# Kernel tuning notes

Hardware: AMD Instinct MI355X
Metric: run time of the kernel (lower is better)

## Reference

```python
import jax, jax.numpy as jnp
import numpy as np

WIN_SIZE = 256
PATCH_SIZE = [8]
CHANNEL = 32
B_CH = 256        # B_outer(8) * CHANNEL(32)
H, E = 8, 64


def _attn(q, k):
    # q, k: [B*ch, L, H, E] -> softmax scores [B*ch, H, L, L]
    scale = 1.0 / jnp.sqrt(jnp.asarray(E, q.dtype))
    scores = jnp.einsum('blhe,bshe->bhls', q, k) * scale
    return jax.nn.softmax(scores, axis=-1)  # dropout is identity in eval


def _channel_mean(a):
    # '(b reduce_b) l m n -> b l m n' mean with reduce_b=CHANNEL (channel innermost)
    bc, h, m, n = a.shape
    return a.reshape(bc // CHANNEL, CHANNEL, h, m, n).mean(axis=1)


def setup_inputs() -> dict:
    key = jax.random.key(0)
    k1, k2, k3, k4 = jax.random.split(key, 4)
    p = PATCH_SIZE[0]
    patch_num = WIN_SIZE // p
    return {
        'queries_patch_size': jax.random.normal(k1, (B_CH, patch_num, H, E), jnp.float32),
        'keys_patch_size':    jax.random.normal(k2, (B_CH, patch_num, H, E), jnp.float32),
        'queries_patch_num':  jax.random.normal(k3, (B_CH, p, H, E), jnp.float32),
        'keys_patch_num':     jax.random.normal(k4, (B_CH, p, H, E), jnp.float32),
        'patch_index': 0,
        'attn_mask': 0,
    }


def reference(queries_patch_size, keys_patch_size, queries_patch_num, keys_patch_num, patch_index, attn_mask):
    p = PATCH_SIZE[patch_index]
    rep = WIN_SIZE // p

    # patch_size branch: element-wise repeat (einops repeat) then channel mean.
    # mean over channel commutes with the repeat, so reduce first (same math,
    # avoids the 536MB intermediate the torch code materializes).
    s_ps = _channel_mean(_attn(queries_patch_size, keys_patch_size))  # [B,H,rep,rep]
    s_ps = jnp.repeat(jnp.repeat(s_ps, p, axis=2), p, axis=3)

    # patch_num branch: torch .repeat == tile, then channel mean (also commutes).
    s_pn = _channel_mean(_attn(queries_patch_num, keys_patch_num))    # [B,H,p,p]
    s_pn = jnp.tile(s_pn, (1, 1, rep, rep))

    return (s_ps, s_pn)
```

## Files before the change

### kernel.cpp

```cpp
#include <hip/hip_runtime.h>
#include <stdint.h>


__global__ __launch_bounds__(256)
void scores_kernel(const float* __restrict__ qps,
                   const float* __restrict__ kps,
                   const float* __restrict__ qpn,
                   const float* __restrict__ kpn,
                   float* __restrict__ ws_ps,
                   float* __restrict__ ws_pn)
{
    __shared__ float red[4][32 * 36];
    const int tid  = threadIdx.x;
    const int wv   = tid >> 6;
    const int lane = tid & 63;
    const int blk  = blockIdx.x;

    if (blk < 512) {
        const int a     = blk >> 3;
        const int chunk = blk & 7;
        const int bo = a >> 3, h = a & 7;
        const int ch = chunk * 4 + wv;
        const int b  = bo * 32 + ch;
        const int i = lane >> 3, j = lane & 7;

        const float4* Q = reinterpret_cast<const float4*>(qps) + ((b * 32 + 4 * i) * 8 + h) * 16;
        const float4* K = reinterpret_cast<const float4*>(kps) + ((b * 32 + 4 * j) * 8 + h) * 16;

        float acc[4][4];
        #pragma unroll
        for (int r = 0; r < 4; ++r)
            #pragma unroll
            for (int c = 0; c < 4; ++c) acc[r][c] = 0.f;

        #pragma unroll 4
        for (int c = 0; c < 16; ++c) {
            float4 q[4], k[4];
            #pragma unroll
            for (int r = 0; r < 4; ++r) { q[r] = Q[r * 128 + c]; k[r] = K[r * 128 + c]; }
            #pragma unroll
            for (int r = 0; r < 4; ++r)
                #pragma unroll
                for (int u = 0; u < 4; ++u) {
                    acc[r][u] = fmaf(q[r].x, k[u].x, acc[r][u]);
                    acc[r][u] = fmaf(q[r].y, k[u].y, acc[r][u]);
                    acc[r][u] = fmaf(q[r].z, k[u].z, acc[r][u]);
                    acc[r][u] = fmaf(q[r].w, k[u].w, acc[r][u]);
                }
        }

        #pragma unroll
        for (int r = 0; r < 4; ++r) {
            float v0 = acc[r][0] * 0.125f, v1 = acc[r][1] * 0.125f;
            float v2 = acc[r][2] * 0.125f, v3 = acc[r][3] * 0.125f;
            float m = fmaxf(fmaxf(v0, v1), fmaxf(v2, v3));
            m = fmaxf(m, __shfl_xor(m, 1));
            m = fmaxf(m, __shfl_xor(m, 2));
            m = fmaxf(m, __shfl_xor(m, 4));
            float e0 = __expf(v0 - m), e1 = __expf(v1 - m);
            float e2 = __expf(v2 - m), e3 = __expf(v3 - m);
            float s = (e0 + e1) + (e2 + e3);
            s += __shfl_xor(s, 1);
            s += __shfl_xor(s, 2);
            s += __shfl_xor(s, 4);
            const float inv = 1.f / (s * 32.f);
            float4 p; p.x = e0 * inv; p.y = e1 * inv; p.z = e2 * inv; p.w = e3 * inv;
            *reinterpret_cast<float4*>(&red[wv][(4 * i + r) * 36 + 4 * j]) = p;
        }
        __syncthreads();

        const int l = tid >> 3, s4 = (tid & 7) * 4;
        const float4 u0 = *reinterpret_cast<const float4*>(&red[0][l * 36 + s4]);
        const float4 u1 = *reinterpret_cast<const float4*>(&red[1][l * 36 + s4]);
        const float4 u2 = *reinterpret_cast<const float4*>(&red[2][l * 36 + s4]);
        const float4 u3 = *reinterpret_cast<const float4*>(&red[3][l * 36 + s4]);
        float4 o;
        o.x = (u0.x + u1.x) + (u2.x + u3.x);
        o.y = (u0.y + u1.y) + (u2.y + u3.y);
        o.z = (u0.z + u1.z) + (u2.z + u3.z);
        o.w = (u0.w + u1.w) + (u2.w + u3.w);
        reinterpret_cast<float4*>(ws_ps + (a * 8 + chunk) * 1024)[tid] = o;
    } else {
        const int bb    = blk - 512;
        const int a2    = bb >> 3;
        const int chunk = bb & 7;
        const int bo = a2 >> 3, h = a2 & 7;
        const int b  = bo * 32 + chunk * 4 + wv;
        const int i = lane >> 3, j = lane & 7;
        const float4* qv = reinterpret_cast<const float4*>(qpn) + ((b * 8 + i) * 8 + h) * 16;
        const float4* kv = reinterpret_cast<const float4*>(kpn) + ((b * 8 + j) * 8 + h) * 16;

        float acc = 0.f;
        #pragma unroll
        for (int c = 0; c < 16; ++c) {
            float4 q = qv[c], k = kv[c];
            acc = fmaf(q.x, k.x, acc);
            acc = fmaf(q.y, k.y, acc);
            acc = fmaf(q.z, k.z, acc);
            acc = fmaf(q.w, k.w, acc);
        }
        const float s = acc * 0.125f;
        float m = s;
        m = fmaxf(m, __shfl_xor(m, 1));
        m = fmaxf(m, __shfl_xor(m, 2));
        m = fmaxf(m, __shfl_xor(m, 4));
        float e = __expf(s - m);
        float sum = e;
        sum += __shfl_xor(sum, 1);
        sum += __shfl_xor(sum, 2);
        sum += __shfl_xor(sum, 4);

        red[wv][lane] = e / (sum * 32.f);
        __syncthreads();
        if (tid < 64) {
            ws_pn[(a2 * 8 + chunk) * 64 + tid] =
                (red[0][tid] + red[1][tid]) + (red[2][tid] + red[3][tid]);
        }
    }
}

__global__ __launch_bounds__(256)
void writer_kernel(const float* __restrict__ ws_ps,
                   const float* __restrict__ ws_pn,
                   float* __restrict__ out)
{
    const int g = blockIdx.x * 256 + threadIdx.x;
    float4* o4 = reinterpret_cast<float4*>(out);
    if (g < 1048576) {
        const int a  = g >> 14;
        const int r  = g & 16383;
        const int i  = r >> 6;
        const int j4 = r & 63;
        const float* base = ws_ps + a * 8192 + (i >> 3) * 32 + (j4 >> 1);
        float v = 0.f;
        #pragma unroll
        for (int k = 0; k < 8; ++k) v += base[k * 1024];
        float4 o; o.x = v; o.y = v; o.z = v; o.w = v;
        o4[g] = o;
    } else {
        const int g2 = g - 1048576;
        const int a  = g2 >> 14;
        const int r  = g2 & 16383;
        const int i  = r >> 6;
        const int j4 = r & 63;
        const float* base = ws_pn + a * 512 + (i & 7) * 8 + 4 * (j4 & 1);
        float4 v = {0.f, 0.f, 0.f, 0.f};
        #pragma unroll
        for (int k = 0; k < 8; ++k) {
            const float4 p = *reinterpret_cast<const float4*>(base + k * 64);
            v.x += p.x; v.y += p.y; v.z += p.z; v.w += p.w;
        }
        o4[g] = v;
    }
}

extern "C" void kernel_launch(void* const* d_in, const int* in_sizes, int n_in,
                              void* d_out, int out_size, void* d_ws, size_t ws_size,
                              hipStream_t stream) {
    const float *qps = nullptr, *kps = nullptr, *qpn = nullptr, *kpn = nullptr;
    for (int idx = 0; idx < n_in; ++idx) {
        if (in_sizes[idx] == 256 * 32 * 8 * 64) {
            if (!qps) qps = (const float*)d_in[idx];
            else if (!kps) kps = (const float*)d_in[idx];
        } else if (in_sizes[idx] == 256 * 8 * 8 * 64) {
            if (!qpn) qpn = (const float*)d_in[idx];
            else if (!kpn) kpn = (const float*)d_in[idx];
        }
    }

    float* ws_ps = (float*)d_ws;
    float* ws_pn = ws_ps + 64 * 8 * 1024;

    scores_kernel<<<1024, 256, 0, stream>>>(qps, kps, qpn, kpn, ws_ps, ws_pn);
    writer_kernel<<<8192, 256, 0, stream>>>(ws_ps, ws_pn, (float*)d_out);
}
```

Before: 120.8 us.

## Split patch-size score tiles into row groups across four times more blocks

Each block of the patch-size scores branch now handles one 8-row group of the 32x32 score matrix, so each thread computes a 1x4 strip instead of a 4x4 tile. The grid grows from 512 to 2048 blocks for that branch, and the shared-memory reduction buffer shrinks to match. The goal is more parallelism and lower register and LDS pressure per block, which should hide memory latency better. The cost is that K rows are loaded four times as often, once per row group.

```diff
diff --git a/kernel.cpp b/kernel.cpp
--- a/kernel.cpp
+++ b/kernel.cpp
@@ -10,78 +10,67 @@
                    float* __restrict__ ws_ps,
                    float* __restrict__ ws_pn)
 {
-    __shared__ float red[4][32 * 36];
+    __shared__ float red[4][8 * 36];
     const int tid  = threadIdx.x;
     const int wv   = tid >> 6;
     const int lane = tid & 63;
     const int blk  = blockIdx.x;
 
-    if (blk < 512) {
-        const int a     = blk >> 3;
-        const int chunk = blk & 7;
+    if (blk < 2048) {
+        const int a     = blk >> 5;
+        const int chunk = (blk >> 2) & 7;
+        const int rg    = blk & 3;
         const int bo = a >> 3, h = a & 7;
-        const int ch = chunk * 4 + wv;
-        const int b  = bo * 32 + ch;
-        const int i = lane >> 3, j = lane & 7;
+        const int b  = bo * 32 + chunk * 4 + wv;
+        const int i2 = lane >> 3;
+        const int j  = lane & 7;
+        const int l  = rg * 8 + i2;
 
-        const float4* Q = reinterpret_cast<const float4*>(qps) + ((b * 32 + 4 * i) * 8 + h) * 16;
+        const float4* Q = reinterpret_cast<const float4*>(qps) + ((b * 32 + l) * 8 + h) * 16;
         const float4* K = reinterpret_cast<const float4*>(kps) + ((b * 32 + 4 * j) * 8 + h) * 16;
 
-        float acc[4][4];
+        float acc[4];
         #pragma unroll
-        for (int r = 0; r < 4; ++r)
-            #pragma unroll
-            for (int c = 0; c < 4; ++c) acc[r][c] = 0.f;
+        for (int u = 0; u < 4; ++u) acc[u] = 0.f;
 
         #pragma unroll 4
         for (int c = 0; c < 16; ++c) {
-            float4 q[4], k[4];
+            const float4 q = Q[c];
+            float4 k[4];
             #pragma unroll
-            for (int r = 0; r < 4; ++r) { q[r] = Q[r * 128 + c]; k[r] = K[r * 128 + c]; }
+            for (int u = 0; u < 4; ++u) k[u] = K[u * 128 + c];
             #pragma unroll
-            for (int r = 0; r < 4; ++r)
-                #pragma unroll
-                for (int u = 0; u < 4; ++u) {
-                    acc[r][u] = fmaf(q[r].x, k[u].x, acc[r][u]);
-                    acc[r][u] = fmaf(q[r].y, k[u].y, acc[r][u]);
-                    acc[r][u] = fmaf(q[r].z, k[u].z, acc[r][u]);
-                    acc[r][u] = fmaf(q[r].w, k[u].w, acc[r][u]);
-                }
+            for (int u = 0; u < 4; ++u) {
+                acc[u] = fmaf(q.x, k[u].x, acc[u]);
+                acc[u] = fmaf(q.y, k[u].y, acc[u]);
+                acc[u] = fmaf(q.z, k[u].z, acc[u]);
+                acc[u] = fmaf(q.w, k[u].w, acc[u]);
+            }
         }
 
-        #pragma unroll
-        for (int r = 0; r < 4; ++r) {
-            float v0 = acc[r][0] * 0.125f, v1 = acc[r][1] * 0.125f;
-            float v2 = acc[r][2] * 0.125f, v3 = acc[r][3] * 0.125f;
-            float m = fmaxf(fmaxf(v0, v1), fmaxf(v2, v3));
-            m = fmaxf(m, __shfl_xor(m, 1));
-            m = fmaxf(m, __shfl_xor(m, 2));
-            m = fmaxf(m, __shfl_xor(m, 4));
-            float e0 = __expf(v0 - m), e1 = __expf(v1 - m);
-            float e2 = __expf(v2 - m), e3 = __expf(v3 - m);
-            float s = (e0 + e1) + (e2 + e3);
-            s += __shfl_xor(s, 1);
-            s += __shfl_xor(s, 2);
-            s += __shfl_xor(s, 4);
-            const float inv = 1.f / (s * 32.f);
-            float4 p; p.x = e0 * inv; p.y = e1 * inv; p.z = e2 * inv; p.w = e3 * inv;
-            *reinterpret_cast<float4*>(&red[wv][(4 * i + r) * 36 + 4 * j]) = p;
-        }
+        float v0 = acc[0] * 0.125f, v1 = acc[1] * 0.125f;
+        float v2 = acc[2] * 0.125f, v3 = acc[3] * 0.125f;
+        float m = fmaxf(fmaxf(v0, v1), fmaxf(v2, v3));
+        m = fmaxf(m, __shfl_xor(m, 1));
+        m = fmaxf(m, __shfl_xor(m, 2));
+        m = fmaxf(m, __shfl_xor(m, 4));
+        float e0 = __expf(v0 - m), e1 = __expf(v1 - m);
+        float e2 = __expf(v2 - m), e3 = __expf(v3 - m);
+        float s = (e0 + e1) + (e2 + e3);
+        s += __shfl_xor(s, 1);
+        s += __shfl_xor(s, 2);
+        s += __shfl_xor(s, 4);
+        const float inv = 1.f / (s * 32.f);
+        float4 p; p.x = e0 * inv; p.y = e1 * inv; p.z = e2 * inv; p.w = e3 * inv;
+        *reinterpret_cast<float4*>(&red[wv][i2 * 36 + 4 * j]) = p;
         __syncthreads();
 
-        const int l = tid >> 3, s4 = (tid & 7) * 4;
-        const float4 u0 = *reinterpret_cast<const float4*>(&red[0][l * 36 + s4]);
-        const float4 u1 = *reinterpret_cast<const float4*>(&red[1][l * 36 + s4]);
-        const float4 u2 = *reinterpret_cast<const float4*>(&red[2][l * 36 + s4]);
-        const float4 u3 = *reinterpret_cast<const float4*>(&red[3][l * 36 + s4]);
-        float4 o;
-        o.x = (u0.x + u1.x) + (u2.x + u3.x);
-        o.y = (u0.y + u1.y) + (u2.y + u3.y);
-        o.z = (u0.z + u1.z) + (u2.z + u3.z);
-        o.w = (u0.w + u1.w) + (u2.w + u3.w);
-        reinterpret_cast<float4*>(ws_ps + (a * 8 + chunk) * 1024)[tid] = o;
+        const int row = tid >> 5, col = tid & 31;
+        const int ad = row * 36 + col;
+        ws_ps[(a * 8 + chunk) * 1024 + rg * 256 + tid] =
+            (red[0][ad] + red[1][ad]) + (red[2][ad] + red[3][ad]);
     } else {
-        const int bb    = blk - 512;
+        const int bb    = blk - 2048;
         const int a2    = bb >> 3;
         const int chunk = bb & 7;
         const int bo = a2 >> 3, h = a2 & 7;
@@ -171,6 +160,6 @@
     float* ws_ps = (float*)d_ws;
     float* ws_pn = ws_ps + 64 * 8 * 1024;
 
-    scores_kernel<<<1024, 256, 0, stream>>>(qps, kps, qpn, kpn, ws_ps, ws_pn);
+    scores_kernel<<<2560, 256, 0, stream>>>(qps, kps, qpn, kpn, ws_ps, ws_pn);
     writer_kernel<<<8192, 256, 0, stream>>>(ws_ps, ws_pn, (float*)d_out);
 }
```

Result: slower. 159.1 us (+31.7%).
